# Performance work log

Hardware: AMD Instinct MI355X
Metric: run time of the kernel (lower is better)

## Reference

```python
import jax, jax.numpy as jnp
import numpy as np

NX, DX, H, DO = 8192, 8, 1024, 1


def setup_inputs() -> dict:
    key = jax.random.key(0)
    ks = jax.random.split(key, 7)
    s1 = 1.0 / np.sqrt(DX)  # torch Linear default init bound
    s2 = 1.0 / np.sqrt(H)
    x = jax.random.normal(ks[0], (NX, DX), jnp.float32)
    W1 = jax.random.uniform(ks[1], (H, DX), jnp.float32, -s1, s1)
    b1 = jax.random.uniform(ks[2], (H,), jnp.float32, -s1, s1)
    W2 = jax.random.uniform(ks[3], (H, H), jnp.float32, -s2, s2)
    b2 = jax.random.uniform(ks[4], (H,), jnp.float32, -s2, s2)
    W3 = jax.random.uniform(ks[5], (DO, H), jnp.float32, -s2, s2)
    b3 = jax.random.uniform(ks[6], (DO,), jnp.float32, -s2, s2)
    return {"x": x, "W1": W1, "b1": b1, "W2": W2, "b2": b2, "W3": W3, "b3": b3}


def reference(x, W1, b1, W2, b2, W3, b3):
    # Forward: Linear -> Tanh -> Linear -> Tanh -> Linear
    z1 = jnp.tanh(x @ W1.T + b1)          # [nx, h]
    z2 = jnp.tanh(z1 @ W2.T + b2)         # [nx, h]
    y = z2 @ W3.T + b3                    # [nx, out]

    # DerivTanh(h) = 4/(e^-h + e^h)^2 = sech^2(h) = 1 - tanh(h)^2
    d1 = 1.0 - z1 * z1                    # [nx, h]
    d2 = 1.0 - z2 * z2                    # [nx, h]

    # Vectorized analytic Jacobian (original loops over each input dim k):
    # tmp_k = d2 * (W2 @ (d1 * W1[:, k]))  then  dydx_k = W3 @ tmp_k
    J = d1[:, :, None] * W1[None, :, :]                    # [nx, h, dx]
    J = d2[:, :, None] * jnp.einsum('ij,njk->nik', W2, J)  # [nx, h, dx]
    dydx = jnp.einsum('oj,njk->nok', W3, J)                # [nx, out, dx]
    # Match original list-of-dx ordering: dydx[k] has shape [nx, out]
    dydx = jnp.transpose(dydx, (2, 0, 1))                  # [dx, nx, out]
    return y, dydx
```

## Files before the change

kernel.cpp:

```cpp
#include <hip/hip_runtime.h>
#include <stdint.h>

#define NXS 8192
#define HS  1024

typedef __attribute__((ext_vector_type(8))) short short8;
typedef __attribute__((ext_vector_type(4))) float f32x4;

__device__ __forceinline__ float bf2f(uint32_t b) {
    union { uint32_t u; float f; } c; c.u = b << 16; return c.f;
}
__device__ __forceinline__ uint16_t f2bf(float f) {
    union { float f; uint32_t u; } c; c.f = f;
    return (uint16_t)((c.u + 0x7fffu + ((c.u >> 16) & 1u)) >> 16);
}
__device__ __forceinline__ void async_cp16(const void* g, void* l) {
    __builtin_amdgcn_global_load_lds(
        (const __attribute__((address_space(1))) void*)g,
        (__attribute__((address_space(3))) void*)l,
        16, 0, 0);
}

__global__ __launch_bounds__(256) void conv_w2(
    const float* __restrict__ W2, uint16_t* __restrict__ W2c,
    uint16_t* __restrict__ W2T, float* __restrict__ yacc)
{
    __shared__ uint16_t tile[64][65];
    const int gid = blockIdx.x * 256 + threadIdx.x;
    if (gid < NXS) yacc[gid] = 0.f;
    const int bx = blockIdx.x & 15, by = blockIdx.x >> 4;
    const int tx = threadIdx.x & 63, ty = threadIdx.x >> 6;
#pragma unroll
    for (int rr = 0; rr < 64; rr += 4) {
        int r = ty + rr;
        uint16_t v = f2bf(W2[(size_t)(by * 64 + r) * HS + bx * 64 + tx]);
        W2c[(size_t)(by * 64 + r) * HS + bx * 64 + tx] = v;
        tile[r][tx] = v;
    }
    __syncthreads();
#pragma unroll
    for (int rr = 0; rr < 64; rr += 4)
        W2T[(size_t)(bx * 64 + ty + rr) * HS + by * 64 + tx] = tile[tx][ty + rr];
}

__global__ __launch_bounds__(256) void k1_z1(
    const float* __restrict__ x, const float* __restrict__ W1,
    const float* __restrict__ b1, uint16_t* __restrict__ Z1)
{
    const int idx = blockIdx.x * 256 + threadIdx.x;
    const int n = idx >> 10, j = idx & 1023;
    float4 x0 = *(const float4*)(x + n * 8);
    float4 x1 = *(const float4*)(x + n * 8 + 4);
    float4 w0 = *(const float4*)(W1 + j * 8);
    float4 w1 = *(const float4*)(W1 + j * 8 + 4);
    float s = b1[j]
        + x0.x * w0.x + x0.y * w0.y + x0.z * w0.z + x0.w * w0.w
        + x1.x * w1.x + x1.y * w1.y + x1.z * w1.z + x1.w * w1.w;
    Z1[idx] = f2bf(tanhf(s));
}

template <int MODE>
__global__ __launch_bounds__(512) void gemm_k(
    const uint16_t* __restrict__ A, const uint16_t* __restrict__ B,
    const float* __restrict__ bias, const float* __restrict__ W3,
    uint16_t* __restrict__ Out, float* __restrict__ yacc)
{
    __shared__ __attribute__((aligned(16))) uint16_t lsA[2][128 * 64];
    __shared__ __attribute__((aligned(16))) uint16_t lsB[2][128 * 64];
    const int t = threadIdx.x;
    const int wave = t >> 6, lane = t & 63;
    const int lq = lane >> 4, lr = lane & 15;
    const int wm = wave >> 1, wn = wave & 1;
    const int rowBase = blockIdx.x * 128;
    const int colBase = blockIdx.y * 128;

    const int s0 = t, s1 = 512 + t;
    const int r0 = s0 >> 3, q0 = (s0 & 7) ^ (r0 & 7);
    const int r1 = s1 >> 3, q1 = (s1 & 7) ^ (r1 & 7);
    const uint16_t* gA0 = A + (size_t)(rowBase + r0) * HS + q0 * 8;
    const uint16_t* gA1 = A + (size_t)(rowBase + r1) * HS + q1 * 8;
    const uint16_t* gB0 = B + (size_t)(colBase + r0) * HS + q0 * 8;
    const uint16_t* gB1 = B + (size_t)(colBase + r1) * HS + q1 * 8;

    f32x4 acc[2][4] = {};

    async_cp16(gA0, (char*)lsA[0] + s0 * 16);
    async_cp16(gA1, (char*)lsA[0] + s1 * 16);
    async_cp16(gB0, (char*)lsB[0] + s0 * 16);
    async_cp16(gB1, (char*)lsB[0] + s1 * 16);
    __syncthreads();

    int buf = 0;
    for (int k0 = 0; k0 < HS; k0 += 64, buf ^= 1) {
        if (k0 + 64 < HS) {
            const int ko = k0 + 64;
            async_cp16(gA0 + ko, (char*)lsA[buf ^ 1] + s0 * 16);
            async_cp16(gA1 + ko, (char*)lsA[buf ^ 1] + s1 * 16);
            async_cp16(gB0 + ko, (char*)lsB[buf ^ 1] + s0 * 16);
            async_cp16(gB1 + ko, (char*)lsB[buf ^ 1] + s1 * 16);
        }
#pragma unroll
        for (int kk = 0; kk < 64; kk += 32) {
            const int kq = (kk >> 3) + lq;
            short8 af[2], bfr[4];
#pragma unroll
            for (int ti = 0; ti < 2; ++ti) {
                int ar = wm * 32 + ti * 16 + lr;
                af[ti] = *(const short8*)((const short*)lsA[buf]
                          + ar * 64 + ((kq ^ (ar & 7)) << 3));
            }
#pragma unroll
            for (int tj = 0; tj < 4; ++tj) {
                int br = wn * 64 + tj * 16 + lr;
                bfr[tj] = *(const short8*)((const short*)lsB[buf]
                          + br * 64 + ((kq ^ (br & 7)) << 3));
            }
#pragma unroll
            for (int ti = 0; ti < 2; ++ti)
#pragma unroll
                for (int tj = 0; tj < 4; ++tj)
                    acc[ti][tj] = __builtin_amdgcn_mfma_f32_16x16x32_bf16(
                        af[ti], bfr[tj], acc[ti][tj], 0, 0, 0);
        }
        __syncthreads();
    }

    if (MODE == 0) {
        float cB[4], cW[4]; int cCol[4];
#pragma unroll
        for (int tj = 0; tj < 4; ++tj) {
            int col = colBase + wn * 64 + tj * 16 + lr;
            cCol[tj] = col;
            cB[tj] = bias[col];
            cW[tj] = W3[col];
        }
#pragma unroll
        for (int ti = 0; ti < 2; ++ti) {
#pragma unroll
            for (int r = 0; r < 4; ++r) {
                int row = rowBase + wm * 32 + ti * 16 + lq * 4 + r;
                float ys = 0.f;
#pragma unroll
                for (int tj = 0; tj < 4; ++tj) {
                    float z2 = tanhf(acc[ti][tj][r] + cB[tj]);
                    ys += z2 * cW[tj];
                    Out[(size_t)row * HS + cCol[tj]] = f2bf((1.f - z2 * z2) * cW[tj]);
                }
                ys += __shfl_xor(ys, 1); ys += __shfl_xor(ys, 2);
                ys += __shfl_xor(ys, 4); ys += __shfl_xor(ys, 8);
                if (lr == 0) atomicAdd(&yacc[row], ys);
            }
        }
    } else {
#pragma unroll
        for (int ti = 0; ti < 2; ++ti)
#pragma unroll
            for (int r = 0; r < 4; ++r) {
                int row = rowBase + wm * 32 + ti * 16 + lq * 4 + r;
#pragma unroll
                for (int tj = 0; tj < 4; ++tj)
                    Out[(size_t)row * HS + colBase + wn * 64 + tj * 16 + lr] =
                        f2bf(acc[ti][tj][r]);
            }
    }
}

__global__ __launch_bounds__(256) void k4_final(
    const float* __restrict__ x, const float* __restrict__ W1,
    const float* __restrict__ b1, const uint16_t* __restrict__ U,
    const float* __restrict__ yacc, const float* __restrict__ b3,
    float* __restrict__ out)
{
    const int n = (blockIdx.x * 256 + threadIdx.x) >> 6;
    const int lane = threadIdx.x & 63;
    float4 x0 = *(const float4*)(x + n * 8);
    float4 x1 = *(const float4*)(x + n * 8 + 4);
    float xf[8] = {x0.x, x0.y, x0.z, x0.w, x1.x, x1.y, x1.z, x1.w};
    float part[8] = {};
    for (int it = 0; it < 16; ++it) {
        int j = it * 64 + lane;
        float u = bf2f(U[(size_t)n * HS + j]);
        float4 w0 = *(const float4*)(W1 + j * 8);
        float4 w1 = *(const float4*)(W1 + j * 8 + 4);
        float wf[8] = {w0.x, w0.y, w0.z, w0.w, w1.x, w1.y, w1.z, w1.w};
        float s = b1[j];
#pragma unroll
        for (int k = 0; k < 8; ++k) s += xf[k] * wf[k];
        float z1 = tanhf(s);
        float c = u * (1.f - z1 * z1);
#pragma unroll
        for (int k = 0; k < 8; ++k) part[k] += c * wf[k];
    }
#pragma unroll
    for (int m = 1; m < 64; m <<= 1)
#pragma unroll
        for (int k = 0; k < 8; ++k) part[k] += __shfl_xor(part[k], m);
    if (lane == 0) {
        out[n] = yacc[n] + b3[0];
#pragma unroll
        for (int k = 0; k < 8; ++k) out[NXS + k * NXS + n] = part[k];
    }
}

extern "C" void kernel_launch(void* const* d_in, const int* in_sizes, int n_in,
                              void* d_out, int out_size, void* d_ws, size_t ws_size,
                              hipStream_t stream) {
    (void)in_sizes; (void)n_in; (void)out_size; (void)ws_size;
    const float* x  = (const float*)d_in[0];
    const float* W1 = (const float*)d_in[1];
    const float* b1 = (const float*)d_in[2];
    const float* W2 = (const float*)d_in[3];
    const float* b2 = (const float*)d_in[4];
    const float* W3 = (const float*)d_in[5];
    const float* b3 = (const float*)d_in[6];
    float* out = (float*)d_out;

    char* ws = (char*)d_ws;
    uint16_t* Z1  = (uint16_t*)(ws);
    uint16_t* U   = (uint16_t*)(ws);
    uint16_t* V   = (uint16_t*)(ws + (size_t)16 * 1024 * 1024);
    uint16_t* W2c = (uint16_t*)(ws + (size_t)32 * 1024 * 1024);
    uint16_t* W2T = (uint16_t*)(ws + (size_t)34 * 1024 * 1024);
    float*    yac = (float*)   (ws + (size_t)36 * 1024 * 1024);

    conv_w2<<<256, 256, 0, stream>>>(W2, W2c, W2T, yac);
    k1_z1<<<NXS * HS / 256, 256, 0, stream>>>(x, W1, b1, Z1);
    gemm_k<0><<<dim3(NXS / 128, HS / 128), 512, 0, stream>>>(Z1, W2c, b2, W3, V, yac);
    gemm_k<1><<<dim3(NXS / 128, HS / 128), 512, 0, stream>>>(V, W2T, nullptr, nullptr, U, nullptr);
    k4_final<<<NXS / 4, 256, 0, stream>>>(x, W1, b1, U, yac, b3, out);
}
```

Baseline: 150.7 us.

## Fuse final Jacobian reduction into second GEMM epilogue with atomics

The second GEMM no longer writes U to global memory. Its epilogue now reads Z1, computes d1*U and reduces against W1 across columns, then atomically accumulates the 8 Jacobian components into a float buffer. This removes the U write and re-read and the recomputation of tanh in the old final kernel. In exchange it adds many atomics, reads Z1 in bf16 instead of recomputing it in fp32, and needs a small output-copy kernel plus zeroing of the buffer. The z1 kernel is also vectorised to compute four outputs per thread with one ushort4 store.

```diff
diff --git a/kernel.cpp b/kernel.cpp
--- a/kernel.cpp
+++ b/kernel.cpp
@@ -23,10 +23,12 @@
 
 __global__ __launch_bounds__(256) void conv_w2(
     const float* __restrict__ W2, uint16_t* __restrict__ W2c,
-    uint16_t* __restrict__ W2T, float* __restrict__ yacc)
+    uint16_t* __restrict__ W2T, float* __restrict__ yacc,
+    float* __restrict__ dacc)
 {
     __shared__ uint16_t tile[64][65];
     const int gid = blockIdx.x * 256 + threadIdx.x;
+    dacc[gid] = 0.f;
     if (gid < NXS) yacc[gid] = 0.f;
     const int bx = blockIdx.x & 15, by = blockIdx.x >> 4;
     const int tx = threadIdx.x & 63, ty = threadIdx.x >> 6;
@@ -47,23 +49,33 @@
     const float* __restrict__ x, const float* __restrict__ W1,
     const float* __restrict__ b1, uint16_t* __restrict__ Z1)
 {
-    const int idx = blockIdx.x * 256 + threadIdx.x;
-    const int n = idx >> 10, j = idx & 1023;
+    const int n = blockIdx.x;
+    const int j = threadIdx.x * 4;
     float4 x0 = *(const float4*)(x + n * 8);
     float4 x1 = *(const float4*)(x + n * 8 + 4);
-    float4 w0 = *(const float4*)(W1 + j * 8);
-    float4 w1 = *(const float4*)(W1 + j * 8 + 4);
-    float s = b1[j]
-        + x0.x * w0.x + x0.y * w0.y + x0.z * w0.z + x0.w * w0.w
-        + x1.x * w1.x + x1.y * w1.y + x1.z * w1.z + x1.w * w1.w;
-    Z1[idx] = f2bf(tanhf(s));
+    float4 bb = *(const float4*)(b1 + j);
+    float sv[4] = {bb.x, bb.y, bb.z, bb.w};
+    ushort4 o;
+    uint16_t* op = (uint16_t*)&o;
+#pragma unroll
+    for (int c = 0; c < 4; ++c) {
+        float4 w0 = *(const float4*)(W1 + (j + c) * 8);
+        float4 w1 = *(const float4*)(W1 + (j + c) * 8 + 4);
+        float s = sv[c]
+            + x0.x * w0.x + x0.y * w0.y + x0.z * w0.z + x0.w * w0.w
+            + x1.x * w1.x + x1.y * w1.y + x1.z * w1.z + x1.w * w1.w;
+        op[c] = f2bf(tanhf(s));
+    }
+    *(ushort4*)(Z1 + (size_t)n * HS + j) = o;
 }
 
 template <int MODE>
 __global__ __launch_bounds__(512) void gemm_k(
     const uint16_t* __restrict__ A, const uint16_t* __restrict__ B,
     const float* __restrict__ bias, const float* __restrict__ W3,
-    uint16_t* __restrict__ Out, float* __restrict__ yacc)
+    uint16_t* __restrict__ Out, float* __restrict__ yacc,
+    const uint16_t* __restrict__ Z1, const float* __restrict__ W1,
+    float* __restrict__ dacc)
 {
     __shared__ __attribute__((aligned(16))) uint16_t lsA[2][128 * 64];
     __shared__ __attribute__((aligned(16))) uint16_t lsB[2][128 * 64];
@@ -125,15 +137,15 @@
         __syncthreads();
     }
 
+    int cCol[4];
+#pragma unroll
+    for (int tj = 0; tj < 4; ++tj)
+        cCol[tj] = colBase + wn * 64 + tj * 16 + lr;
+
     if (MODE == 0) {
-        float cB[4], cW[4]; int cCol[4];
-#pragma unroll
-        for (int tj = 0; tj < 4; ++tj) {
-            int col = colBase + wn * 64 + tj * 16 + lr;
-            cCol[tj] = col;
-            cB[tj] = bias[col];
-            cW[tj] = W3[col];
-        }
+        float cB[4], cW[4];
+#pragma unroll
+        for (int tj = 0; tj < 4; ++tj) { cB[tj] = bias[cCol[tj]]; cW[tj] = W3[cCol[tj]]; }
 #pragma unroll
         for (int ti = 0; ti < 2; ++ti) {
 #pragma unroll
@@ -153,53 +165,43 @@
         }
     } else {
 #pragma unroll
-        for (int ti = 0; ti < 2; ++ti)
+        for (int ti = 0; ti < 2; ++ti) {
 #pragma unroll
             for (int r = 0; r < 4; ++r) {
                 int row = rowBase + wm * 32 + ti * 16 + lq * 4 + r;
-#pragma unroll
-                for (int tj = 0; tj < 4; ++tj)
-                    Out[(size_t)row * HS + colBase + wn * 64 + tj * 16 + lr] =
-                        f2bf(acc[ti][tj][r]);
-            }
-    }
-}
-
-__global__ __launch_bounds__(256) void k4_final(
-    const float* __restrict__ x, const float* __restrict__ W1,
-    const float* __restrict__ b1, const uint16_t* __restrict__ U,
-    const float* __restrict__ yacc, const float* __restrict__ b3,
-    float* __restrict__ out)
-{
-    const int n = (blockIdx.x * 256 + threadIdx.x) >> 6;
-    const int lane = threadIdx.x & 63;
-    float4 x0 = *(const float4*)(x + n * 8);
-    float4 x1 = *(const float4*)(x + n * 8 + 4);
-    float xf[8] = {x0.x, x0.y, x0.z, x0.w, x1.x, x1.y, x1.z, x1.w};
-    float part[8] = {};
-    for (int it = 0; it < 16; ++it) {
-        int j = it * 64 + lane;
-        float u = bf2f(U[(size_t)n * HS + j]);
-        float4 w0 = *(const float4*)(W1 + j * 8);
-        float4 w1 = *(const float4*)(W1 + j * 8 + 4);
-        float wf[8] = {w0.x, w0.y, w0.z, w0.w, w1.x, w1.y, w1.z, w1.w};
-        float s = b1[j];
-#pragma unroll
-        for (int k = 0; k < 8; ++k) s += xf[k] * wf[k];
-        float z1 = tanhf(s);
-        float c = u * (1.f - z1 * z1);
-#pragma unroll
-        for (int k = 0; k < 8; ++k) part[k] += c * wf[k];
-    }
-#pragma unroll
-    for (int m = 1; m < 64; m <<= 1)
-#pragma unroll
-        for (int k = 0; k < 8; ++k) part[k] += __shfl_xor(part[k], m);
-    if (lane == 0) {
-        out[n] = yacc[n] + b3[0];
-#pragma unroll
-        for (int k = 0; k < 8; ++k) out[NXS + k * NXS + n] = part[k];
-    }
+                float pk[8] = {};
+#pragma unroll
+                for (int tj = 0; tj < 4; ++tj) {
+                    float z1 = bf2f(Z1[(size_t)row * HS + cCol[tj]]);
+                    float c = acc[ti][tj][r] * (1.f - z1 * z1);
+                    float4 w0 = *(const float4*)(W1 + cCol[tj] * 8);
+                    float4 w1 = *(const float4*)(W1 + cCol[tj] * 8 + 4);
+                    pk[0] += c * w0.x; pk[1] += c * w0.y;
+                    pk[2] += c * w0.z; pk[3] += c * w0.w;
+                    pk[4] += c * w1.x; pk[5] += c * w1.y;
+                    pk[6] += c * w1.z; pk[7] += c * w1.w;
+                }
+#pragma unroll
+                for (int m = 1; m < 16; m <<= 1)
+#pragma unroll
+                    for (int k = 0; k < 8; ++k) pk[k] += __shfl_xor(pk[k], m);
+                if (lr == 0) {
+#pragma unroll
+                    for (int k = 0; k < 8; ++k)
+                        atomicAdd(&dacc[k * NXS + row], pk[k]);
+                }
+            }
+        }
+    }
+}
+
+__global__ __launch_bounds__(256) void k5_out(
+    const float* __restrict__ yacc, const float* __restrict__ dacc,
+    const float* __restrict__ b3, float* __restrict__ out)
+{
+    const int idx = blockIdx.x * 256 + threadIdx.x;
+    if (idx < NXS) out[idx] = yacc[idx] + b3[0];
+    else           out[idx] = dacc[idx - NXS];
 }
 
 extern "C" void kernel_launch(void* const* d_in, const int* in_sizes, int n_in,
@@ -217,15 +219,17 @@
 
     char* ws = (char*)d_ws;
     uint16_t* Z1  = (uint16_t*)(ws);
-    uint16_t* U   = (uint16_t*)(ws);
     uint16_t* V   = (uint16_t*)(ws + (size_t)16 * 1024 * 1024);
     uint16_t* W2c = (uint16_t*)(ws + (size_t)32 * 1024 * 1024);
     uint16_t* W2T = (uint16_t*)(ws + (size_t)34 * 1024 * 1024);
     float*    yac = (float*)   (ws + (size_t)36 * 1024 * 1024);
-
-    conv_w2<<<256, 256, 0, stream>>>(W2, W2c, W2T, yac);
-    k1_z1<<<NXS * HS / 256, 256, 0, stream>>>(x, W1, b1, Z1);
-    gemm_k<0><<<dim3(NXS / 128, HS / 128), 512, 0, stream>>>(Z1, W2c, b2, W3, V, yac);
-    gemm_k<1><<<dim3(NXS / 128, HS / 128), 512, 0, stream>>>(V, W2T, nullptr, nullptr, U, nullptr);
-    k4_final<<<NXS / 4, 256, 0, stream>>>(x, W1, b1, U, yac, b3, out);
-}
+    float*    dac = (float*)   (ws + (size_t)36 * 1024 * 1024 + 32768);
+
+    conv_w2<<<256, 256, 0, stream>>>(W2, W2c, W2T, yac, dac);
+    k1_z1<<<NXS, 256, 0, stream>>>(x, W1, b1, Z1);
+    gemm_k<0><<<dim3(NXS / 128, HS / 128), 512, 0, stream>>>(
+        Z1, W2c, b2, W3, V, yac, nullptr, nullptr, nullptr);
+    gemm_k<1><<<dim3(NXS / 128, HS / 128), 512, 0, stream>>>(
+        V, W2T, nullptr, nullptr, nullptr, nullptr, Z1, W1, dac);
+    k5_out<<<(NXS * 9 + 255) / 256, 256, 0, stream>>>(yac, dac, b3, out);
+}
```

Result: slower. 165.6 us (+9.9%).
